# Optimization experiments

Measured on AMD Instinct MI355X. Metric: run time of the kernel, lower is better.

Reference implementation:

```python
import jax, jax.numpy as jnp
import numpy as np

ALPHA = 0.5
NEG_MASK = 1000000.0


def setup_inputs() -> dict:
    key = jax.random.key(0)
    k1, k2, k3, k4 = jax.random.split(key, 4)
    B, Dv, Nq, Ns, D = 64, 1024, 32, 1024, 128
    return {
        "q_single": jax.random.normal(k1, (B, Dv), dtype=jnp.float32),
        "d_single": jax.random.normal(k2, (B, Dv), dtype=jnp.float32),
        "q_multi": jax.random.normal(k3, (B, Nq, D), dtype=jnp.float32),
        "d_multi": jax.random.normal(k4, (B, Ns, D), dtype=jnp.float32),
    }


def _single_vector_loss(q_single, d_single):
    # scores: [B, B]
    scores = jnp.einsum('bd,cd->bc', q_single, d_single)
    # MatryoshkaCELoss iterates rows of scores; each row is CE'd against its
    # diagonal target and the per-row losses are summed (relative_importance=None -> ones).
    logp = jax.nn.log_softmax(scores, axis=-1)
    return -jnp.sum(jnp.diagonal(logp))


def _multi_vector_loss(q_multi, d_multi):
    B = q_multi.shape[0]
    # [B, B, Nq, Ns] late-interaction score tensor -> max over doc tokens, sum over query tokens
    sim = jnp.einsum('bnd,csd->bcns', q_multi, d_multi)
    scores = jnp.sum(jnp.max(sim, axis=3), axis=2)  # [B, B]
    pos_scores = jnp.diagonal(scores)
    neg_scores = jnp.max(scores - jnp.eye(B, dtype=scores.dtype) * NEG_MASK, axis=1)
    return jnp.mean(jax.nn.softplus(neg_scores - pos_scores))


def reference(q_single, d_single, q_multi, d_multi):
    sv = _single_vector_loss(q_single, d_single)
    mv = _multi_vector_loss(q_multi, d_multi)
    return ALPHA * sv + (1.0 - ALPHA) * mv
```

## Files before the change

kernel.cpp:

```cpp
#include <hip/hip_runtime.h>
#include <hip/hip_bf16.h>
#include <math.h>

#define BSZ 64
#define DV  1024
#define NQ  32
#define NS  1024
#define DD  128

#define ALPHA 0.5f

typedef __attribute__((ext_vector_type(8))) int   int8v;
typedef __attribute__((ext_vector_type(4))) float floatx4;
#define SCALE1 127

__global__ void prep_kernel(const float* __restrict__ qm, const float* __restrict__ dm,
                            const float* __restrict__ qs, const float* __restrict__ ds,
                            unsigned char* __restrict__ qb8, unsigned char* __restrict__ db8,
                            float* __restrict__ svrow) {
    __shared__ float row[BSZ];
    int bid = blockIdx.x, t = threadIdx.x;
    int w = t >> 6, l = t & 63;
    int lane16 = l & 15, quad = (l >> 4) & 3;

    auto cvt_chunk = [&](const float* src, unsigned char* dst) {
        int dw[8];
#pragma unroll
        for (int j = 0; j < 8; ++j) {
            float4 v = ((const float4*)src)[j];
            int d0 = __builtin_amdgcn_cvt_pk_fp8_f32(v.x, v.y, 0, false);
            dw[j]  = __builtin_amdgcn_cvt_pk_fp8_f32(v.z, v.w, d0, true);
        }
        ((int4*)dst)[0] = make_int4(dw[0], dw[1], dw[2], dw[3]);
        ((int4*)dst)[1] = make_int4(dw[4], dw[5], dw[6], dw[7]);
    };

    if (bid < 256) {
        int gw = bid * 4 + w;
#pragma unroll
        for (int it = 0; it < 4; ++it) {
            int ch = gw + it * 1024;
            int c = ch >> 6, st = ch & 63;
            const float* src = dm + ((size_t)(c * NS + st * 16 + lane16)) * DD + quad * 32;
            cvt_chunk(src, db8 + (size_t)ch * 2048 + l * 32);
        }
    } else if (bid < 264) {
        int gw = (bid - 256) * 4 + w;
#pragma unroll
        for (int it = 0; it < 4; ++it) {
            int ch = gw * 4 + it;
            int b = ch >> 1, nt = ch & 1;
            const float* src = qm + ((size_t)(b * NQ + nt * 16 + lane16)) * DD + quad * 32;
            cvt_chunk(src, qb8 + (size_t)ch * 2048 + l * 32);
        }
    } else {
        int b = bid - 264;
        int c = t >> 2, part = t & 3;
        const float4* qv = (const float4*)(qs + b * DV);
        const float4* dv = (const float4*)(ds + c * DV);
        float acc = 0.f;
        int k0 = part * 64;
#pragma unroll 8
        for (int k = k0; k < k0 + 64; ++k) {
            float4 a = qv[k], bb = dv[k];
            acc += a.x * bb.x + a.y * bb.y + a.z * bb.z + a.w * bb.w;
        }
        acc += __shfl_xor(acc, 1);
        acc += __shfl_xor(acc, 2);
        if (part == 0) row[c] = acc;
        __syncthreads();
        if (t < BSZ) {
            float v = row[t];
            float m = v;
#pragma unroll
            for (int o = 1; o < 64; o <<= 1) m = fmaxf(m, __shfl_xor(m, o));
            float e = expf(v - m);
#pragma unroll
            for (int o = 1; o < 64; o <<= 1) e += __shfl_xor(e, o);
            float lse = m + logf(e);
            if (t == 0) svrow[b] = lse - row[b];
        }
    }
}

__launch_bounds__(256, 2)
__global__ void multi_kernel(const unsigned char* __restrict__ qb8,
                             const unsigned char* __restrict__ db8,
                             float* __restrict__ scores) {
    int bid = blockIdx.x;
    int x = bid & 7, rr = bid >> 3;
    int c  = x * 8 + (rr & 7);
    int bg = rr >> 3;
    int t  = threadIdx.x;
    int w  = t >> 6;
    int l  = t & 63;
    int lane16 = l & 15;
    int quad   = (l >> 4) & 3;

    __shared__ float smax[4][4][NQ];

    int8v af[4][2];
#pragma unroll
    for (int bi = 0; bi < 4; ++bi)
#pragma unroll
        for (int nt = 0; nt < 2; ++nt)
            af[bi][nt] = *(const int8v*)(qb8 +
                (size_t)(((bg * 4 + bi) * 2 + nt) * 2048) + l * 32);

    float mx[4][2][4];
#pragma unroll
    for (int bi = 0; bi < 4; ++bi)
#pragma unroll
        for (int nt = 0; nt < 2; ++nt)
#pragma unroll
            for (int r = 0; r < 4; ++r) mx[bi][nt][r] = -1e30f;

    int8v bf[2];
    auto loadb = [&](int which, int st) {
        bf[which] = *(const int8v*)(db8 + (size_t)((c * 64 + st) * 2048) + l * 32);
    };

    loadb(0, w);
#pragma unroll
    for (int i = 0; i < 16; ++i) {
        if (i < 15) loadb((i + 1) & 1, w + (i + 1) * 4);
        int8v B = bf[i & 1];
#pragma unroll
        for (int bi = 0; bi < 4; ++bi)
#pragma unroll
            for (int nt = 0; nt < 2; ++nt) {
                floatx4 acc = __builtin_amdgcn_mfma_scale_f32_16x16x128_f8f6f4(
                    af[bi][nt], B, (floatx4){0.f, 0.f, 0.f, 0.f},
                    0, 0,
                    0, SCALE1,
                    0, SCALE1);
#pragma unroll
                for (int r = 0; r < 4; ++r)
                    mx[bi][nt][r] = fmaxf(mx[bi][nt][r], acc[r]);
            }
    }

#pragma unroll
    for (int bi = 0; bi < 4; ++bi)
#pragma unroll
        for (int nt = 0; nt < 2; ++nt)
#pragma unroll
            for (int r = 0; r < 4; ++r) {
                float v = mx[bi][nt][r];
                v = fmaxf(v, __shfl_xor(v, 1));
                v = fmaxf(v, __shfl_xor(v, 2));
                v = fmaxf(v, __shfl_xor(v, 4));
                v = fmaxf(v, __shfl_xor(v, 8));
                mx[bi][nt][r] = v;
            }
    if (lane16 == 0) {
#pragma unroll
        for (int bi = 0; bi < 4; ++bi)
#pragma unroll
            for (int nt = 0; nt < 2; ++nt)
#pragma unroll
                for (int r = 0; r < 4; ++r)
                    smax[w][bi][nt * 16 + quad * 4 + r] = mx[bi][nt][r];
    }
    __syncthreads();
    if (t < 4 * NQ) {
        int bi = t >> 5, n = t & 31;
        float v = fmaxf(fmaxf(smax[0][bi][n], smax[1][bi][n]),
                        fmaxf(smax[2][bi][n], smax[3][bi][n]));
#pragma unroll
        for (int o = 1; o < 32; o <<= 1) v += __shfl_xor(v, o);
        if (n == 0) scores[(bg * 4 + bi) * BSZ + c] = v;
    }
}

__global__ void finish_kernel(const float* __restrict__ scores, const float* __restrict__ svrow,
                              float* __restrict__ out) {
    int t = threadIdx.x;
    float pos = scores[t * BSZ + t];
    float neg = -1e30f;
    for (int cc = 0; cc < BSZ; ++cc)
        if (cc != t) neg = fmaxf(neg, scores[t * BSZ + cc]);
    float xx = neg - pos;
    float sp = fmaxf(xx, 0.f) + log1pf(expf(-fabsf(xx)));
    float sv = svrow[t];
#pragma unroll
    for (int o = 1; o < 64; o <<= 1) {
        sp += __shfl_xor(sp, o);
        sv += __shfl_xor(sv, o);
    }
    if (t == 0) out[0] = ALPHA * sv + (1.0f - ALPHA) * (sp * (1.0f / BSZ));
}

extern "C" void kernel_launch(void* const* d_in, const int* in_sizes, int n_in,
                              void* d_out, int out_size, void* d_ws, size_t ws_size,
                              hipStream_t stream) {
    const float* q_single = (const float*)d_in[0];
    const float* d_single = (const float*)d_in[1];
    const float* q_multi  = (const float*)d_in[2];
    const float* d_multi  = (const float*)d_in[3];
    float* out = (float*)d_out;

    unsigned char* qb8 = (unsigned char*)d_ws;
    unsigned char* db8 = (unsigned char*)d_ws + 262144;
    float* scores      = (float*)((char*)d_ws + 262144 + 8388608);
    float* svrow       = (float*)((char*)d_ws + 262144 + 8388608 + 16384);

    prep_kernel<<<328, 256, 0, stream>>>(q_multi, d_multi, q_single, d_single,
                                         qb8, db8, svrow);
    multi_kernel<<<1024, 256, 0, stream>>>(qb8, db8, scores);
    finish_kernel<<<1, 64, 0, stream>>>(scores, svrow, out);
}
```

Before: 121.4 us.

## Fuse fp8 conversion into the MFMA kernel and double queries per block

Drops the separate prep pass that wrote fp8 copies of the multi-vector inputs to global memory. Each block now converts its 8 query rows into LDS and converts doc tiles to fp8 in registers straight from fp32 global loads, with a one-tile register prefetch. Blocks now cover 8 query batches instead of 4, so the grid shrinks to 512 MFMA blocks plus 64 single-vector blocks, and one launch plus the intermediate round trip goes away. In exchange each doc tile is read as fp32 (4x the bytes) by 8 blocks, register pressure rises with 16 A fragments and 64 accumulators, and conversion ALU work now sits on the MFMA critical path.

```diff
diff --git a/kernel.cpp b/kernel.cpp
--- a/kernel.cpp
+++ b/kernel.cpp
@@ -1,5 +1,4 @@
 #include <hip/hip_runtime.h>
-#include <hip/hip_bf16.h>
 #include <math.h>
 
 #define BSZ 64
@@ -14,47 +13,19 @@
 typedef __attribute__((ext_vector_type(4))) float floatx4;
 #define SCALE1 127
 
-__global__ void prep_kernel(const float* __restrict__ qm, const float* __restrict__ dm,
-                            const float* __restrict__ qs, const float* __restrict__ ds,
-                            unsigned char* __restrict__ qb8, unsigned char* __restrict__ db8,
-                            float* __restrict__ svrow) {
+__launch_bounds__(256, 2)
+__global__ void fused_kernel(const float* __restrict__ qm, const float* __restrict__ dm,
+                             const float* __restrict__ qs, const float* __restrict__ ds,
+                             float* __restrict__ scores, float* __restrict__ svrow) {
+    __shared__ __align__(32) unsigned char lds_q[16 * 2048];
+    __shared__ float lds_smax[4][8][32];
     __shared__ float row[BSZ];
-    int bid = blockIdx.x, t = threadIdx.x;
-    int w = t >> 6, l = t & 63;
-    int lane16 = l & 15, quad = (l >> 4) & 3;
 
-    auto cvt_chunk = [&](const float* src, unsigned char* dst) {
-        int dw[8];
-#pragma unroll
-        for (int j = 0; j < 8; ++j) {
-            float4 v = ((const float4*)src)[j];
-            int d0 = __builtin_amdgcn_cvt_pk_fp8_f32(v.x, v.y, 0, false);
-            dw[j]  = __builtin_amdgcn_cvt_pk_fp8_f32(v.z, v.w, d0, true);
-        }
-        ((int4*)dst)[0] = make_int4(dw[0], dw[1], dw[2], dw[3]);
-        ((int4*)dst)[1] = make_int4(dw[4], dw[5], dw[6], dw[7]);
-    };
+    int bid = blockIdx.x;
+    int t = threadIdx.x;
 
-    if (bid < 256) {
-        int gw = bid * 4 + w;
-#pragma unroll
-        for (int it = 0; it < 4; ++it) {
-            int ch = gw + it * 1024;
-            int c = ch >> 6, st = ch & 63;
-            const float* src = dm + ((size_t)(c * NS + st * 16 + lane16)) * DD + quad * 32;
-            cvt_chunk(src, db8 + (size_t)ch * 2048 + l * 32);
-        }
-    } else if (bid < 264) {
-        int gw = (bid - 256) * 4 + w;
-#pragma unroll
-        for (int it = 0; it < 4; ++it) {
-            int ch = gw * 4 + it;
-            int b = ch >> 1, nt = ch & 1;
-            const float* src = qm + ((size_t)(b * NQ + nt * 16 + lane16)) * DD + quad * 32;
-            cvt_chunk(src, qb8 + (size_t)ch * 2048 + l * 32);
-        }
-    } else {
-        int b = bid - 264;
+    if (bid >= 512) {
+        int b = bid - 512;
         int c = t >> 2, part = t & 3;
         const float4* qv = (const float4*)(qs + b * DV);
         const float4* dv = (const float4*)(ds + c * DV);
@@ -80,57 +51,73 @@
             float lse = m + logf(e);
             if (t == 0) svrow[b] = lse - row[b];
         }
+        return;
     }
-}
 
-__launch_bounds__(256, 2)
-__global__ void multi_kernel(const unsigned char* __restrict__ qb8,
-                             const unsigned char* __restrict__ db8,
-                             float* __restrict__ scores) {
-    int bid = blockIdx.x;
     int x = bid & 7, rr = bid >> 3;
     int c  = x * 8 + (rr & 7);
     int bg = rr >> 3;
-    int t  = threadIdx.x;
-    int w  = t >> 6;
-    int l  = t & 63;
-    int lane16 = l & 15;
-    int quad   = (l >> 4) & 3;
+    int w = t >> 6, l = t & 63;
+    int lane16 = l & 15, quad = (l >> 4) & 3;
 
-    __shared__ float smax[4][4][NQ];
+#pragma unroll
+    for (int k = 0; k < 4; ++k) {
+        int ch = w * 4 + k;
+        int bi = ch >> 1, nt = ch & 1;
+        const float* src = qm + ((size_t)((bg * 8 + bi) * NQ + nt * 16 + lane16)) * DD + quad * 32;
+        int dw[8];
+#pragma unroll
+        for (int j = 0; j < 8; ++j) {
+            float4 v = ((const float4*)src)[j];
+            int d0 = __builtin_amdgcn_cvt_pk_fp8_f32(v.x, v.y, 0, false);
+            dw[j]  = __builtin_amdgcn_cvt_pk_fp8_f32(v.z, v.w, d0, true);
+        }
+        int4* dst = (int4*)(lds_q + ch * 2048 + l * 32);
+        dst[0] = make_int4(dw[0], dw[1], dw[2], dw[3]);
+        dst[1] = make_int4(dw[4], dw[5], dw[6], dw[7]);
+    }
+    __syncthreads();
 
-    int8v af[4][2];
+    int8v af[8][2];
 #pragma unroll
-    for (int bi = 0; bi < 4; ++bi)
+    for (int bi = 0; bi < 8; ++bi)
 #pragma unroll
         for (int nt = 0; nt < 2; ++nt)
-            af[bi][nt] = *(const int8v*)(qb8 +
-                (size_t)(((bg * 4 + bi) * 2 + nt) * 2048) + l * 32);
+            af[bi][nt] = *(const int8v*)(lds_q + (bi * 2 + nt) * 2048 + l * 32);
 
-    float mx[4][2][4];
+    float mx[8][2][4];
 #pragma unroll
-    for (int bi = 0; bi < 4; ++bi)
+    for (int bi = 0; bi < 8; ++bi)
 #pragma unroll
         for (int nt = 0; nt < 2; ++nt)
 #pragma unroll
             for (int r = 0; r < 4; ++r) mx[bi][nt][r] = -1e30f;
 
-    int8v bf[2];
-    auto loadb = [&](int which, int st) {
-        bf[which] = *(const int8v*)(db8 + (size_t)((c * 64 + st) * 2048) + l * 32);
-    };
+    const float* dcur = dm + ((size_t)(c * NS + w * 16 + lane16)) * DD + quad * 32;
+    float4 raw[8];
+#pragma unroll
+    for (int j = 0; j < 8; ++j) raw[j] = ((const float4*)dcur)[j];
+    const float* dnext = dcur + 4 * 16 * DD;
 
-    loadb(0, w);
+#pragma unroll 1
+    for (int i = 0; i < 16; ++i) {
+        int8v bf;
 #pragma unroll
-    for (int i = 0; i < 16; ++i) {
-        if (i < 15) loadb((i + 1) & 1, w + (i + 1) * 4);
-        int8v B = bf[i & 1];
+        for (int j = 0; j < 8; ++j) {
+            int d0 = __builtin_amdgcn_cvt_pk_fp8_f32(raw[j].x, raw[j].y, 0, false);
+            bf[j]  = __builtin_amdgcn_cvt_pk_fp8_f32(raw[j].z, raw[j].w, d0, true);
+        }
+        if (i < 15) {
 #pragma unroll
-        for (int bi = 0; bi < 4; ++bi)
+            for (int j = 0; j < 8; ++j) raw[j] = ((const float4*)dnext)[j];
+            dnext += 4 * 16 * DD;
+        }
+#pragma unroll
+        for (int bi = 0; bi < 8; ++bi)
 #pragma unroll
             for (int nt = 0; nt < 2; ++nt) {
                 floatx4 acc = __builtin_amdgcn_mfma_scale_f32_16x16x128_f8f6f4(
-                    af[bi][nt], B, (floatx4){0.f, 0.f, 0.f, 0.f},
+                    af[bi][nt], bf, (floatx4){0.f, 0.f, 0.f, 0.f},
                     0, 0,
                     0, SCALE1,
                     0, SCALE1);
@@ -141,7 +128,7 @@
     }
 
 #pragma unroll
-    for (int bi = 0; bi < 4; ++bi)
+    for (int bi = 0; bi < 8; ++bi)
 #pragma unroll
         for (int nt = 0; nt < 2; ++nt)
 #pragma unroll
@@ -155,21 +142,21 @@
             }
     if (lane16 == 0) {
 #pragma unroll
-        for (int bi = 0; bi < 4; ++bi)
+        for (int bi = 0; bi < 8; ++bi)
 #pragma unroll
             for (int nt = 0; nt < 2; ++nt)
 #pragma unroll
                 for (int r = 0; r < 4; ++r)
-                    smax[w][bi][nt * 16 + quad * 4 + r] = mx[bi][nt][r];
+                    lds_smax[w][bi][nt * 16 + quad * 4 + r] = mx[bi][nt][r];
     }
     __syncthreads();
-    if (t < 4 * NQ) {
+    {
         int bi = t >> 5, n = t & 31;
-        float v = fmaxf(fmaxf(smax[0][bi][n], smax[1][bi][n]),
-                        fmaxf(smax[2][bi][n], smax[3][bi][n]));
+        float v = fmaxf(fmaxf(lds_smax[0][bi][n], lds_smax[1][bi][n]),
+                        fmaxf(lds_smax[2][bi][n], lds_smax[3][bi][n]));
 #pragma unroll
         for (int o = 1; o < 32; o <<= 1) v += __shfl_xor(v, o);
-        if (n == 0) scores[(bg * 4 + bi) * BSZ + c] = v;
+        if (n == 0) scores[(bg * 8 + bi) * BSZ + c] = v;
     }
 }
 
@@ -200,13 +187,10 @@
     const float* d_multi  = (const float*)d_in[3];
     float* out = (float*)d_out;
 
-    unsigned char* qb8 = (unsigned char*)d_ws;
-    unsigned char* db8 = (unsigned char*)d_ws + 262144;
-    float* scores      = (float*)((char*)d_ws + 262144 + 8388608);
-    float* svrow       = (float*)((char*)d_ws + 262144 + 8388608 + 16384);
+    float* scores = (float*)d_ws;
+    float* svrow  = (float*)((char*)d_ws + 16384);
 
-    prep_kernel<<<328, 256, 0, stream>>>(q_multi, d_multi, q_single, d_single,
-                                         qb8, db8, svrow);
-    multi_kernel<<<1024, 256, 0, stream>>>(qb8, db8, scores);
+    fused_kernel<<<576, 256, 0, stream>>>(q_multi, d_multi, q_single, d_single,
+                                          scores, svrow);
     finish_kernel<<<1, 64, 0, stream>>>(scores, svrow, out);
 }
```

After: 153.3 us. 26.2% more time.

## Fuse finish into multi kernel via last-block atomic, rebalance prep grid

Applied to the files above, without the earlier changes.

Removes the separate single-block finish kernel: each multi_kernel block increments an atomic counter and the last block computes the final loss from scores and svrow. The prep kernel now runs the single-vector rows first and spreads the doc fp8 conversion over 1024 blocks with one chunk per wave, not four, for more parallelism. It also prefetches two B tiles ahead in the MFMA loop. Together these cut a kernel launch and tail latency, at the cost of an atomic plus threadfence in every block, and the counter reset depends on prep having finished first.

```diff
diff --git a/kernel.cpp b/kernel.cpp
--- a/kernel.cpp
+++ b/kernel.cpp
@@ -1,5 +1,4 @@
 #include <hip/hip_runtime.h>
-#include <hip/hip_bf16.h>
 #include <math.h>
 
 #define BSZ 64
@@ -17,7 +16,7 @@
 __global__ void prep_kernel(const float* __restrict__ qm, const float* __restrict__ dm,
                             const float* __restrict__ qs, const float* __restrict__ ds,
                             unsigned char* __restrict__ qb8, unsigned char* __restrict__ db8,
-                            float* __restrict__ svrow) {
+                            float* __restrict__ svrow, unsigned int* __restrict__ cnt) {
     __shared__ float row[BSZ];
     int bid = blockIdx.x, t = threadIdx.x;
     int w = t >> 6, l = t & 63;
@@ -35,26 +34,8 @@
         ((int4*)dst)[1] = make_int4(dw[4], dw[5], dw[6], dw[7]);
     };
 
-    if (bid < 256) {
-        int gw = bid * 4 + w;
-#pragma unroll
-        for (int it = 0; it < 4; ++it) {
-            int ch = gw + it * 1024;
-            int c = ch >> 6, st = ch & 63;
-            const float* src = dm + ((size_t)(c * NS + st * 16 + lane16)) * DD + quad * 32;
-            cvt_chunk(src, db8 + (size_t)ch * 2048 + l * 32);
-        }
-    } else if (bid < 264) {
-        int gw = (bid - 256) * 4 + w;
-#pragma unroll
-        for (int it = 0; it < 4; ++it) {
-            int ch = gw * 4 + it;
-            int b = ch >> 1, nt = ch & 1;
-            const float* src = qm + ((size_t)(b * NQ + nt * 16 + lane16)) * DD + quad * 32;
-            cvt_chunk(src, qb8 + (size_t)ch * 2048 + l * 32);
-        }
-    } else {
-        int b = bid - 264;
+    if (bid < 64) {
+        int b = bid;
         int c = t >> 2, part = t & 3;
         const float4* qv = (const float4*)(qs + b * DV);
         const float4* dv = (const float4*)(ds + c * DV);
@@ -80,13 +61,31 @@
             float lse = m + logf(e);
             if (t == 0) svrow[b] = lse - row[b];
         }
+    } else if (bid < 72) {
+        if (bid == 64 && t == 0) *cnt = 0;
+        int gw = (bid - 64) * 4 + w;
+#pragma unroll
+        for (int it = 0; it < 4; ++it) {
+            int ch = gw * 4 + it;
+            int b = ch >> 1, nt = ch & 1;
+            const float* src = qm + ((size_t)(b * NQ + nt * 16 + lane16)) * DD + quad * 32;
+            cvt_chunk(src, qb8 + (size_t)ch * 2048 + l * 32);
+        }
+    } else {
+        int ch = (bid - 72) * 4 + w;
+        int c = ch >> 6, st = ch & 63;
+        const float* src = dm + ((size_t)(c * NS + st * 16 + lane16)) * DD + quad * 32;
+        cvt_chunk(src, db8 + (size_t)ch * 2048 + l * 32);
     }
 }
 
 __launch_bounds__(256, 2)
 __global__ void multi_kernel(const unsigned char* __restrict__ qb8,
                              const unsigned char* __restrict__ db8,
-                             float* __restrict__ scores) {
+                             float* __restrict__ scores,
+                             const float* __restrict__ svrow,
+                             unsigned int* __restrict__ cnt,
+                             float* __restrict__ out) {
     int bid = blockIdx.x;
     int x = bid & 7, rr = bid >> 3;
     int c  = x * 8 + (rr & 7);
@@ -98,6 +97,7 @@
     int quad   = (l >> 4) & 3;
 
     __shared__ float smax[4][4][NQ];
+    __shared__ int is_last;
 
     int8v af[4][2];
 #pragma unroll
@@ -121,10 +121,11 @@
     };
 
     loadb(0, w);
+    loadb(1, w + 4);
 #pragma unroll
     for (int i = 0; i < 16; ++i) {
-        if (i < 15) loadb((i + 1) & 1, w + (i + 1) * 4);
         int8v B = bf[i & 1];
+        if (i + 2 < 16) loadb(i & 1, w + (i + 2) * 4);
 #pragma unroll
         for (int bi = 0; bi < 4; ++bi)
 #pragma unroll
@@ -171,24 +172,29 @@
         for (int o = 1; o < 32; o <<= 1) v += __shfl_xor(v, o);
         if (n == 0) scores[(bg * 4 + bi) * BSZ + c] = v;
     }
-}
-
-__global__ void finish_kernel(const float* __restrict__ scores, const float* __restrict__ svrow,
-                              float* __restrict__ out) {
-    int t = threadIdx.x;
-    float pos = scores[t * BSZ + t];
-    float neg = -1e30f;
-    for (int cc = 0; cc < BSZ; ++cc)
-        if (cc != t) neg = fmaxf(neg, scores[t * BSZ + cc]);
-    float xx = neg - pos;
-    float sp = fmaxf(xx, 0.f) + log1pf(expf(-fabsf(xx)));
-    float sv = svrow[t];
-#pragma unroll
-    for (int o = 1; o < 64; o <<= 1) {
-        sp += __shfl_xor(sp, o);
-        sv += __shfl_xor(sv, o);
-    }
-    if (t == 0) out[0] = ALPHA * sv + (1.0f - ALPHA) * (sp * (1.0f / BSZ));
+
+    __threadfence();
+    __syncthreads();
+    if (t == 0) is_last = (atomicAdd(cnt, 1u) == 1023u);
+    __syncthreads();
+    if (is_last) {
+        __threadfence();
+        if (t < 64) {
+            float pos = scores[t * BSZ + t];
+            float neg = -1e30f;
+            for (int cc = 0; cc < BSZ; ++cc)
+                if (cc != t) neg = fmaxf(neg, scores[t * BSZ + cc]);
+            float xx = neg - pos;
+            float sp = fmaxf(xx, 0.f) + log1pf(expf(-fabsf(xx)));
+            float sv = svrow[t];
+#pragma unroll
+            for (int o = 1; o < 64; o <<= 1) {
+                sp += __shfl_xor(sp, o);
+                sv += __shfl_xor(sv, o);
+            }
+            if (t == 0) out[0] = ALPHA * sv + (1.0f - ALPHA) * (sp * (1.0f / BSZ));
+        }
+    }
 }
 
 extern "C" void kernel_launch(void* const* d_in, const int* in_sizes, int n_in,
@@ -204,9 +210,9 @@
     unsigned char* db8 = (unsigned char*)d_ws + 262144;
     float* scores      = (float*)((char*)d_ws + 262144 + 8388608);
     float* svrow       = (float*)((char*)d_ws + 262144 + 8388608 + 16384);
-
-    prep_kernel<<<328, 256, 0, stream>>>(q_multi, d_multi, q_single, d_single,
-                                         qb8, db8, svrow);
-    multi_kernel<<<1024, 256, 0, stream>>>(qb8, db8, scores);
-    finish_kernel<<<1, 64, 0, stream>>>(scores, svrow, out);
+    unsigned int* cnt  = (unsigned int*)((char*)d_ws + 262144 + 8388608 + 16384 + 256);
+
+    prep_kernel<<<1096, 256, 0, stream>>>(q_multi, d_multi, q_single, d_single,
+                                          qb8, db8, svrow, cnt);
+    multi_kernel<<<1024, 256, 0, stream>>>(qb8, db8, scores, svrow, cnt, out);
 }
```

Measured after the change: 181.5 us. +49.5%, slower.
